# Optimization experiments

Measured on AMD Instinct MI355X. Metric: run time of the kernel, lower is better.

Reference implementation:

```python
import jax, jax.numpy as jnp
import numpy as np

N = 100000   # nodes
E = 1600000  # edges
IN = 128     # input_dim
H = 64       # hidden_dim
OUT = 2      # output_dim
G = 64       # number of graphs in the batch


def setup_inputs() -> dict:
    key = jax.random.key(0)
    ks = jax.random.split(key, 12)
    x = jax.random.normal(ks[0], (N, IN), dtype=jnp.float32)
    edge_index = jax.random.randint(ks[1], (2, E), 0, N, dtype=jnp.int64)
    batch = jnp.sort(jax.random.randint(ks[2], (N,), 0, G, dtype=jnp.int64))
    s = 0.05
    return {
        "x": x,
        "edge_index": edge_index,
        "batch": batch,
        "W1": jax.random.normal(ks[3], (IN, H), dtype=jnp.float32) * s,
        "b1": jnp.zeros((H,), dtype=jnp.float32),
        "W2": jax.random.normal(ks[4], (H, H), dtype=jnp.float32) * s,
        "b2": jnp.zeros((H,), dtype=jnp.float32),
        "W3": jax.random.normal(ks[5], (H, H), dtype=jnp.float32) * s,
        "b3": jnp.zeros((H,), dtype=jnp.float32),
        "Wm1": jax.random.normal(ks[6], (H, H), dtype=jnp.float32) * s,
        "bm1": jnp.zeros((H,), dtype=jnp.float32),
        "Wm2": jax.random.normal(ks[7], (H, OUT), dtype=jnpp.float32) * s if False else jax.random.normal(ks[7], (H, OUT), dtype=jnp.float32) * s,
        "bm2": jnp.zeros((OUT,), dtype=jnp.float32),
    }


def _gcn_conv(x, W, b, src, dst, norm, n_nodes):
    # PyG GCNConv: h = x @ W; message = norm * h[src]; scatter-add at dst; + bias
    h = x @ W                                  # [N, H]
    msg = h[src] * norm[:, None]               # [E+N, H] gather + scale
    out = jax.ops.segment_sum(msg, dst, num_segments=n_nodes)
    return out + b


def reference(x, edge_index, batch, W1, b1, W2, b2, W3, b3, Wm1, bm1, Wm2, bm2):
    n = x.shape[0]
    # add self-loops (PyG GCNConv default add_self_loops=True)
    loop = jnp.arange(n, dtype=edge_index.dtype)
    src = jnp.concatenate([edge_index[0], loop])
    dst = jnp.concatenate([edge_index[1], loop])
    # symmetric normalization deg^-1/2 (deg over target nodes, incl. self-loops)
    deg = jax.ops.segment_sum(jnp.ones_like(dst, dtype=x.dtype), dst, num_segments=n)
    dinv = jnp.where(deg > 0, jax.lax.rsqrt(deg), 0.0)
    norm = dinv[src] * dinv[dst]               # [E+N]

    h = jax.nn.relu(_gcn_conv(x, W1, b1, src, dst, norm, n))   # dropout: eval -> identity
    h = jax.nn.relu(_gcn_conv(h, W2, b2, src, dst, norm, n))
    h = jax.nn.relu(_gcn_conv(h, W3, b3, src, dst, norm, n))

    # global_mean_pool over batch ids
    sums = jax.ops.segment_sum(h, batch, num_segments=G)       # [G, H]
    cnts = jax.ops.segment_sum(jnp.ones((n,), dtype=h.dtype), batch, num_segments=G)
    pooled = sums / jnp.maximum(cnts, 1.0)[:, None]

    # MLP head: Linear -> ReLU -> (Dropout eval) -> Linear
    z = jax.nn.relu(pooled @ Wm1 + bm1)
    return z @ Wm2 + bm2                                       # [G, OUT]
```

## Files before the change

### kernel.cpp

```cpp
#include <hip/hip_runtime.h>
#include <hip/hip_bf16.h>

#define NNODES 100000
#define NEDGES 1600000
#define IND 128
#define HD 64
#define OUTD 2
#define NG 64
#define SCAN_CHUNK 1024
#define BINSHIFT 9
#define BINSZ 512
#define PB 256

typedef __attribute__((ext_vector_type(8))) short short8v;
typedef __attribute__((ext_vector_type(4))) float floatx4;

static __device__ __forceinline__ unsigned short f2bf(float f) {
    __hip_bfloat16 h = __float2bfloat16(f);
    return *(unsigned short*)&h;
}
static __device__ __forceinline__ float bf2f(unsigned short u) {
    __hip_bfloat16 h = *(__hip_bfloat16*)&u;
    return __bfloat162float(h);
}

__global__ __launch_bounds__(256) void binA_kernel(const int* __restrict__ dst,
                                                   int* __restrict__ bbc,
                                                   int E, int nbins) {
    __shared__ int lh[256];
    lh[threadIdx.x] = 0;
    __syncthreads();
    int ebpb = (E + PB - 1) / PB;
    int e0 = blockIdx.x * ebpb;
    int e1 = min(e0 + ebpb, E);
    for (int e = e0 + threadIdx.x; e < e1; e += 256)
        atomicAdd(&lh[dst[e] >> BINSHIFT], 1);
    __syncthreads();
    bbc[blockIdx.x * 256 + threadIdx.x] = lh[threadIdx.x];
}

__global__ __launch_bounds__(256) void binB1_kernel(int* __restrict__ bbc,
                                                    int* __restrict__ binTotal,
                                                    int* __restrict__ binStart) {
    __shared__ int ws[4];
    int b = blockIdx.x;
    int t = threadIdx.x, lane = t & 63, wv = t >> 6;
    int v = bbc[t * 256 + b];
    int sc = v;
#pragma unroll
    for (int d = 1; d < 64; d <<= 1) { int u = __shfl_up(sc, d, 64); if (lane >= d) sc += u; }
    if (lane == 63) ws[wv] = sc;
    __syncthreads();
    int add = 0;
    for (int w = 0; w < wv; w++) add += ws[w];
    bbc[t * 256 + b] = sc - v + add;
    if (t == 255) { int tot = sc + add; binTotal[b] = tot; binStart[b] = tot; }
}

__global__ __launch_bounds__(64) void scan_bsums_kernel(int* __restrict__ bsum, int nchunks) {
    int lane = threadIdx.x;
    int cpl = (nchunks + 63) / 64;
    int vals[8];
    int i0 = lane * cpl;
    int t = 0;
    for (int k = 0; k < cpl; k++) {
        int i = i0 + k;
        vals[k] = (i < nchunks) ? bsum[i] : 0;
        t += vals[k];
    }
    int sc = t;
#pragma unroll
    for (int d = 1; d < 64; d <<= 1) { int v = __shfl_up(sc, d, 64); if (lane >= d) sc += v; }
    int ex = sc - t;
    for (int k = 0; k < cpl; k++) {
        int i = i0 + k;
        if (i < nchunks) bsum[i] = ex;
        ex += vals[k];
    }
}

__global__ __launch_bounds__(256) void binC_kernel(const int* __restrict__ src,
                                                   const int* __restrict__ dst,
                                                   const int* __restrict__ bbc,
                                                   const int* __restrict__ binStart,
                                                   unsigned int* __restrict__ binned,
                                                   int E, int nbins) {
    __shared__ int cur[256];
    int t = threadIdx.x;
    if (t < nbins) cur[t] = binStart[t] + bbc[blockIdx.x * 256 + t];
    __syncthreads();
    int ebpb = (E + PB - 1) / PB;
    int e0 = blockIdx.x * ebpb;
    int e1 = min(e0 + ebpb, E);
    for (int e = e0 + t; e < e1; e += 256) {
        int d = dst[e];
        int b = d >> BINSHIFT;
        int p = atomicAdd(&cur[b], 1);
        binned[p] = ((unsigned int)(d & (BINSZ - 1)) << 17) | (unsigned int)src[e];
    }
}

__global__ __launch_bounds__(256) void binH_kernel(const unsigned int* __restrict__ binned,
                                                   const int* __restrict__ binStart,
                                                   const int* __restrict__ binTotal,
                                                   int* __restrict__ hist,
                                                   float* __restrict__ dinv, int n) {
    __shared__ int dh[BINSZ];
    int b = blockIdx.x;
    int t = threadIdx.x;
    dh[t] = 0; dh[t + 256] = 0;
    __syncthreads();
    int s0 = binStart[b], cnt = binTotal[b];
    for (int i = t; i < cnt; i += 256)
        atomicAdd(&dh[binned[s0 + i] >> 17], 1);
    __syncthreads();
#pragma unroll
    for (int r = 0; r < 2; r++) {
        int i = t + r * 256;
        int node = (b << BINSHIFT) + i;
        if (node < n) {
            int dg = dh[i];
            hist[node] = dg;
            dinv[node] = 1.0f / sqrtf((float)(dg + 1));
        }
    }
}

__global__ __launch_bounds__(256) void scan_sum_kernel(const int* __restrict__ hist,
                                                       int* __restrict__ bsum, int n) {
    __shared__ int wsums[4];
    int lane = threadIdx.x & 63, wv = threadIdx.x >> 6;
    int i0 = blockIdx.x * SCAN_CHUNK + threadIdx.x * 4;
    int t = 0;
#pragma unroll
    for (int k = 0; k < 4; k++) { int i = i0 + k; if (i < n) t += hist[i]; }
#pragma unroll
    for (int d = 32; d > 0; d >>= 1) t += __shfl_down(t, d, 64);
    if (lane == 0) wsums[wv] = t;
    __syncthreads();
    if (threadIdx.x == 0) bsum[blockIdx.x] = wsums[0] + wsums[1] + wsums[2] + wsums[3];
}

__global__ __launch_bounds__(256) void scan_write_kernel(const int* __restrict__ hist,
                                                         const int* __restrict__ bofs,
                                                         int* __restrict__ rowptr,
                                                         int n, int total) {
    __shared__ int wsum[4];
    int lane = threadIdx.x & 63, wv = threadIdx.x >> 6;
    int i0 = blockIdx.x * SCAN_CHUNK + threadIdx.x * 4;
    int h[4]; int t = 0;
#pragma unroll
    for (int k = 0; k < 4; k++) { int i = i0 + k; h[k] = (i < n) ? hist[i] : 0; t += h[k]; }
    int sc = t;
#pragma unroll
    for (int d = 1; d < 64; d <<= 1) { int v = __shfl_up(sc, d, 64); if (lane >= d) sc += v; }
    if (lane == 63) wsum[wv] = sc;
    __syncthreads();
    int wofs = 0;
    for (int w = 0; w < wv; w++) wofs += wsum[w];
    int ex = (sc - t) + wofs + bofs[blockIdx.x];
#pragma unroll
    for (int k = 0; k < 4; k++) { int i = i0 + k; if (i < n) rowptr[i] = ex; ex += h[k]; }
    if (blockIdx.x == 0 && threadIdx.x == 0) rowptr[n] = total;
}

__global__ __launch_bounds__(256) void binD_kernel(const unsigned int* __restrict__ binned,
                                                   const int* __restrict__ binStart,
                                                   const int* __restrict__ binTotal,
                                                   const int* __restrict__ hist,
                                                   const int* __restrict__ rowptr,
                                                   int* __restrict__ ssrc, int n) {
    __shared__ int cntL[BINSZ];
    __shared__ int rpL[BINSZ];
    int b = blockIdx.x;
    int t = threadIdx.x;
#pragma unroll
    for (int r = 0; r < 2; r++) {
        int i = t + r * 256;
        int node = (b << BINSHIFT) + i;
        if (node < n) { cntL[i] = hist[node]; rpL[i] = rowptr[node]; }
    }
    __syncthreads();
    int s0 = binStart[b], cnt = binTotal[b];
    for (int i = t; i < cnt; i += 256) {
        unsigned int rec = binned[s0 + i];
        int doff = rec >> 17;
        int s = rec & 0x1FFFF;
        int idx = atomicSub(&cntL[doff], 1) - 1;
        ssrc[rpL[doff] + idx] = s;
    }
}

__global__ __launch_bounds__(256) void cvtWT_kernel(const float* __restrict__ W,
                                                    unsigned short* __restrict__ WT, int K) {
    int i = blockIdx.x * 256 + threadIdx.x;
    if (i < 64 * K) {
        int n = i / K, k = i - n * K;
        WT[i] = f2bf(W[k * 64 + n]);
    }
}

template <int K, bool BF16IN>
__global__ __launch_bounds__(256) void mm_mfma_kernel(const void* __restrict__ Xv,
                                                      const unsigned short* __restrict__ WT,
                                                      const float* __restrict__ dinv,
                                                      unsigned short* __restrict__ Tb, int nn) {
    const int lane = threadIdx.x & 63;
    const int wv   = threadIdx.x >> 6;
    const int nb   = blockIdx.x * 64 + wv * 16;
    if (nb >= nn) return;
    const int col  = lane & 15;
    const int quad = lane >> 4;
    const int m    = min(nb + col, nn - 1);

    floatx4 acc0 = {0.f, 0.f, 0.f, 0.f};
    floatx4 acc1 = {0.f, 0.f, 0.f, 0.f};
    floatx4 acc2 = {0.f, 0.f, 0.f, 0.f};
    floatx4 acc3 = {0.f, 0.f, 0.f, 0.f};

#pragma unroll
    for (int ks = 0; ks < K; ks += 32) {
        const int k0 = ks + quad * 8;
        short8v a;
        if (BF16IN) {
            a = *(const short8v*)((const unsigned short*)Xv + (size_t)m * K + k0);
        } else {
            const float* xr = (const float*)Xv + (size_t)m * K + k0;
            float4 f0 = *(const float4*)(xr);
            float4 f1 = *(const float4*)(xr + 4);
            a[0] = (short)f2bf(f0.x); a[1] = (short)f2bf(f0.y);
            a[2] = (short)f2bf(f0.z); a[3] = (short)f2bf(f0.w);
            a[4] = (short)f2bf(f1.x); a[5] = (short)f2bf(f1.y);
            a[6] = (short)f2bf(f1.z); a[7] = (short)f2bf(f1.w);
        }
        short8v b0 = *(const short8v*)(WT + (size_t)(0  + col) * K + k0);
        short8v b1 = *(const short8v*)(WT + (size_t)(16 + col) * K + k0);
        short8v b2 = *(const short8v*)(WT + (size_t)(32 + col) * K + k0);
        short8v b3 = *(const short8v*)(WT + (size_t)(48 + col) * K + k0);
        acc0 = __builtin_amdgcn_mfma_f32_16x16x32_bf16(a, b0, acc0, 0, 0, 0);
        acc1 = __builtin_amdgcn_mfma_f32_16x16x32_bf16(a, b1, acc1, 0, 0, 0);
        acc2 = __builtin_amdgcn_mfma_f32_16x16x32_bf16(a, b2, acc2, 0, 0, 0);
        acc3 = __builtin_amdgcn_mfma_f32_16x16x32_bf16(a, b3, acc3, 0, 0, 0);
    }

#pragma unroll
    for (int r = 0; r < 4; r++) {
        int node = nb + quad * 4 + r;
        if (node < nn) {
            float sc = dinv[node];
            unsigned short* o = Tb + (size_t)node * 64 + col;
            o[0]  = f2bf(sc * acc0[r]);
            o[16] = f2bf(sc * acc1[r]);
            o[32] = f2bf(sc * acc2[r]);
            o[48] = f2bf(sc * acc3[r]);
        }
    }
}

__global__ __launch_bounds__(256) void agg_kernel(const unsigned short* __restrict__ Tb,
                                                  const int* __restrict__ rowptr,
                                                  const int* __restrict__ ssrc,
                                                  const float* __restrict__ dinv,
                                                  const float* __restrict__ bias,
                                                  unsigned short* __restrict__ Ob, int nn) {
    int wave = __builtin_amdgcn_readfirstlane((blockIdx.x * 256 + threadIdx.x) >> 6);
    int lane = threadIdx.x & 63;
    if (wave >= nn) return;
    int n = wave;
    float acc = bf2f(Tb[(size_t)n * 64 + lane]);
    int rb = rowptr[n], re = rowptr[n + 1];
    int i = rb;
    for (; i + 16 <= re; i += 16) {
        int s[16];
#pragma unroll
        for (int k = 0; k < 16; k++) s[k] = ssrc[i + k];
        float v[16];
#pragma unroll
        for (int k = 0; k < 16; k++) v[k] = bf2f(Tb[(size_t)s[k] * 64 + lane]);
#pragma unroll
        for (int k = 0; k < 16; k++) acc += v[k];
    }
    for (; i + 4 <= re; i += 4) {
        int s0 = ssrc[i], s1 = ssrc[i + 1], s2 = ssrc[i + 2], s3 = ssrc[i + 3];
        float v0 = bf2f(Tb[(size_t)s0 * 64 + lane]);
        float v1 = bf2f(Tb[(size_t)s1 * 64 + lane]);
        float v2 = bf2f(Tb[(size_t)s2 * 64 + lane]);
        float v3 = bf2f(Tb[(size_t)s3 * 64 + lane]);
        acc += v0; acc += v1; acc += v2; acc += v3;
    }
    for (; i < re; i++)
        acc += bf2f(Tb[(size_t)ssrc[i] * 64 + lane]);
    float o = dinv[n] * acc + bias[lane];
    o = o > 0.f ? o : 0.f;
    Ob[(size_t)n * 64 + lane] = f2bf(o);
}

__global__ __launch_bounds__(256) void pool_kernel(const unsigned short* __restrict__ Hb,
                                                   const int* __restrict__ batch,
                                                   float* __restrict__ pooled,
                                                   float* __restrict__ gcnt, int nn) {
    int wid = (blockIdx.x * 256 + threadIdx.x) >> 6;
    int lane = threadIdx.x & 63;
    int nwaves = (gridDim.x * 256) >> 6;
    int per = (nn + nwaves - 1) / nwaves;
    int n0 = wid * per;
    int n1 = n0 + per; if (n1 > nn) n1 = nn;
    if (n0 >= n1) return;
    int cur = batch[n0];
    float acc = 0.f, cnt = 0.f;
    for (int n = n0; n < n1; ++n) {
        int g = batch[n];
        if (g != cur) {
            atomicAdd(&pooled[cur * 64 + lane], acc);
            if (lane == 0) atomicAdd(&gcnt[cur], cnt);
            acc = 0.f; cnt = 0.f; cur = g;
        }
        acc += bf2f(Hb[(size_t)n * 64 + lane]);
        cnt += 1.f;
    }
    atomicAdd(&pooled[cur * 64 + lane], acc);
    if (lane == 0) atomicAdd(&gcnt[cur], cnt);
}

__global__ __launch_bounds__(256) void head_kernel(const float* __restrict__ pooled,
                                                   const float* __restrict__ gcnt,
                                                   const float* __restrict__ Wm1,
                                                   const float* __restrict__ bm1,
                                                   const float* __restrict__ Wm2,
                                                   const float* __restrict__ bm2,
                                                   float* __restrict__ out) {
    __shared__ float P[NG * 64];
    __shared__ float Z[NG * 64];
    int tid = threadIdx.x;
    for (int i = tid; i < NG * 64; i += 256) {
        int g = i >> 6;
        float c = gcnt[g];
        c = c > 1.f ? c : 1.f;
        P[i] = pooled[i] / c;
    }
    __syncthreads();
    for (int i = tid; i < NG * 64; i += 256) {
        int g = i >> 6, j = i & 63;
        float a = bm1[j];
#pragma unroll 8
        for (int k = 0; k < 64; ++k) a += P[g * 64 + k] * Wm1[k * 64 + j];
        Z[i] = a > 0.f ? a : 0.f;
    }
    __syncthreads();
    for (int i = tid; i < NG * OUTD; i += 256) {
        int g = i / OUTD, o = i % OUTD;
        float a = bm2[o];
#pragma unroll 8
        for (int k = 0; k < 64; ++k) a += Z[g * 64 + k] * Wm2[k * OUTD + o];
        out[i] = a;
    }
}

extern "C" void kernel_launch(void* const* d_in, const int* in_sizes, int n_in,
                              void* d_out, int out_size, void* d_ws, size_t ws_size,
                              hipStream_t stream) {
    const float* x    = (const float*)d_in[0];
    const int*  edge  = (const int*)d_in[1];
    const int*  batch = (const int*)d_in[2];
    const float* W1 = (const float*)d_in[3];
    const float* b1 = (const float*)d_in[4];
    const float* W2 = (const float*)d_in[5];
    const float* b2 = (const float*)d_in[6];
    const float* W3 = (const float*)d_in[7];
    const float* b3 = (const float*)d_in[8];
    const float* Wm1 = (const float*)d_in[9];
    const float* bm1 = (const float*)d_in[10];
    const float* Wm2 = (const float*)d_in[11];
    const float* bm2 = (const float*)d_in[12];

    const int N_ = in_sizes[2];
    const int E_ = in_sizes[1] / 2;
    const int* src = edge;
    const int* dst = edge + E_;
    const int nbins = (N_ + BINSZ - 1) >> BINSHIFT;

    char* w = (char*)d_ws;
    auto alloc = [&](size_t bytes) -> void* {
        void* p = (void*)w;
        w += (bytes + 255) & ~(size_t)255;
        return p;
    };
    float* dinv   = (float*)alloc((size_t)N_ * 4);
    int*   hist   = (int*)alloc((size_t)N_ * 4);
    int*   rowptr = (int*)alloc((size_t)(N_ + 1) * 4);
    int*   bsum   = (int*)alloc(512 * 4);
    int*   bbc    = (int*)alloc((size_t)256 * 256 * 4);
    int*   binTotal = (int*)alloc(256 * 4);
    int*   binStart = (int*)alloc(256 * 4);
    int*   ssrc   = (int*)alloc((size_t)E_ * 4);
    unsigned int* binned = (unsigned int*)alloc((size_t)E_ * 4);
    unsigned short* Tb  = (unsigned short*)alloc((size_t)N_ * 64 * 2);
    unsigned short* hBb = (unsigned short*)alloc((size_t)N_ * 64 * 2);
    unsigned short* WT1 = (unsigned short*)alloc((size_t)64 * IND * 2);
    unsigned short* WT2 = (unsigned short*)alloc((size_t)64 * HD * 2);
    unsigned short* WT3 = (unsigned short*)alloc((size_t)64 * HD * 2);
    float* pooled = (float*)alloc((size_t)(NG * 64 + NG) * 4);
    float* gcnt   = pooled + NG * 64;

    const int nchunks = (N_ + SCAN_CHUNK - 1) / SCAN_CHUNK;

    hipMemsetAsync(pooled, 0, (size_t)(NG * 64 + NG) * 4, stream);

    binA_kernel<<<PB, 256, 0, stream>>>(dst, bbc, E_, nbins);
    binB1_kernel<<<nbins, 256, 0, stream>>>(bbc, binTotal, binStart);
    scan_bsums_kernel<<<1, 64, 0, stream>>>(binStart, nbins);
    binC_kernel<<<PB, 256, 0, stream>>>(src, dst, bbc, binStart, binned, E_, nbins);
    binH_kernel<<<nbins, 256, 0, stream>>>(binned, binStart, binTotal, hist, dinv, N_);
    scan_sum_kernel<<<nchunks, 256, 0, stream>>>(hist, bsum, N_);
    scan_bsums_kernel<<<1, 64, 0, stream>>>(bsum, nchunks);
    scan_write_kernel<<<nchunks, 256, 0, stream>>>(hist, bsum, rowptr, N_, E_);
    binD_kernel<<<nbins, 256, 0, stream>>>(binned, binStart, binTotal, hist, rowptr, ssrc, N_);

    cvtWT_kernel<<<(64 * IND + 255) / 256, 256, 0, stream>>>(W1, WT1, IND);
    cvtWT_kernel<<<(64 * HD + 255) / 256, 256, 0, stream>>>(W2, WT2, HD);
    cvtWT_kernel<<<(64 * HD + 255) / 256, 256, 0, stream>>>(W3, WT3, HD);

    const int mmblk = (N_ + 63) / 64;
    const int aggblk = (N_ + 3) / 4;

    mm_mfma_kernel<IND, false><<<mmblk, 256, 0, stream>>>(x, WT1, dinv, Tb, N_);
    agg_kernel<<<aggblk, 256, 0, stream>>>(Tb, rowptr, ssrc, dinv, b1, hBb, N_);
    mm_mfma_kernel<HD, true><<<mmblk, 256, 0, stream>>>(hBb, WT2, dinv, Tb, N_);
    agg_kernel<<<aggblk, 256, 0, stream>>>(Tb, rowptr, ssrc, dinv, b2, hBb, N_);
    mm_mfma_kernel<HD, true><<<mmblk, 256, 0, stream>>>(hBb, WT3, dinv, Tb, N_);
    agg_kernel<<<aggblk, 256, 0, stream>>>(Tb, rowptr, ssrc, dinv, b3, hBb, N_);

    pool_kernel<<<256, 256, 0, stream>>>(hBb, batch, pooled, gcnt, N_);
    head_kernel<<<1, 256, 0, stream>>>(pooled, gcnt, Wm1, bm1, Wm2, bm2, (float*)d_out);
}
```

Measured before the change: 411.0 us.

## Fuse degree histogram, CSR scan and edge scatter into one per-bin kernel

Since edges are already bucketed by destination bin, and bin offsets are known from binStart, each bin block now computes the degree histogram, a local exclusive scan for rowptr, dinv, and the final scatter of sources into CSR order, all in one kernel. This replaces the separate hist, two-pass global scan and binD kernels, removing several launches and the round trips of hist/rowptr through global memory. The three weight-transpose kernels are also merged into one launch. In exchange, each bin block does more serial work.

```diff
diff --git a/kernel.cpp b/kernel.cpp
--- a/kernel.cpp
+++ b/kernel.cpp
@@ -7,7 +7,6 @@
 #define HD 64
 #define OUTD 2
 #define NG 64
-#define SCAN_CHUNK 1024
 #define BINSHIFT 9
 #define BINSZ 512
 #define PB 256
@@ -100,14 +99,18 @@
     }
 }
 
-__global__ __launch_bounds__(256) void binH_kernel(const unsigned int* __restrict__ binned,
-                                                   const int* __restrict__ binStart,
-                                                   const int* __restrict__ binTotal,
-                                                   int* __restrict__ hist,
-                                                   float* __restrict__ dinv, int n) {
+__global__ __launch_bounds__(256) void binHD_kernel(const unsigned int* __restrict__ binned,
+                                                    const int* __restrict__ binStart,
+                                                    const int* __restrict__ binTotal,
+                                                    float* __restrict__ dinv,
+                                                    int* __restrict__ rowptr,
+                                                    int* __restrict__ ssrc,
+                                                    int n, int E) {
     __shared__ int dh[BINSZ];
-    int b = blockIdx.x;
-    int t = threadIdx.x;
+    __shared__ int rp[BINSZ];
+    __shared__ int wsum[4];
+    int b = blockIdx.x, t = threadIdx.x;
+    int lane = t & 63, wv = t >> 6;
     dh[t] = 0; dh[t + 256] = 0;
     __syncthreads();
     int s0 = binStart[b], cnt = binTotal[b];
@@ -118,85 +121,56 @@
     for (int r = 0; r < 2; r++) {
         int i = t + r * 256;
         int node = (b << BINSHIFT) + i;
-        if (node < n) {
-            int dg = dh[i];
-            hist[node] = dg;
-            dinv[node] = 1.0f / sqrtf((float)(dg + 1));
-        }
-    }
-}
-
-__global__ __launch_bounds__(256) void scan_sum_kernel(const int* __restrict__ hist,
-                                                       int* __restrict__ bsum, int n) {
-    __shared__ int wsums[4];
-    int lane = threadIdx.x & 63, wv = threadIdx.x >> 6;
-    int i0 = blockIdx.x * SCAN_CHUNK + threadIdx.x * 4;
-    int t = 0;
-#pragma unroll
-    for (int k = 0; k < 4; k++) { int i = i0 + k; if (i < n) t += hist[i]; }
-#pragma unroll
-    for (int d = 32; d > 0; d >>= 1) t += __shfl_down(t, d, 64);
-    if (lane == 0) wsums[wv] = t;
-    __syncthreads();
-    if (threadIdx.x == 0) bsum[blockIdx.x] = wsums[0] + wsums[1] + wsums[2] + wsums[3];
-}
-
-__global__ __launch_bounds__(256) void scan_write_kernel(const int* __restrict__ hist,
-                                                         const int* __restrict__ bofs,
-                                                         int* __restrict__ rowptr,
-                                                         int n, int total) {
-    __shared__ int wsum[4];
-    int lane = threadIdx.x & 63, wv = threadIdx.x >> 6;
-    int i0 = blockIdx.x * SCAN_CHUNK + threadIdx.x * 4;
-    int h[4]; int t = 0;
-#pragma unroll
-    for (int k = 0; k < 4; k++) { int i = i0 + k; h[k] = (i < n) ? hist[i] : 0; t += h[k]; }
-    int sc = t;
+        if (node < n) dinv[node] = 1.0f / sqrtf((float)(dh[i] + 1));
+    }
+    int d0 = dh[2 * t], d1 = dh[2 * t + 1];
+    int p = d0 + d1;
+    int sc = p;
 #pragma unroll
     for (int d = 1; d < 64; d <<= 1) { int v = __shfl_up(sc, d, 64); if (lane >= d) sc += v; }
     if (lane == 63) wsum[wv] = sc;
     __syncthreads();
-    int wofs = 0;
-    for (int w = 0; w < wv; w++) wofs += wsum[w];
-    int ex = (sc - t) + wofs + bofs[blockIdx.x];
-#pragma unroll
-    for (int k = 0; k < 4; k++) { int i = i0 + k; if (i < n) rowptr[i] = ex; ex += h[k]; }
-    if (blockIdx.x == 0 && threadIdx.x == 0) rowptr[n] = total;
-}
-
-__global__ __launch_bounds__(256) void binD_kernel(const unsigned int* __restrict__ binned,
-                                                   const int* __restrict__ binStart,
-                                                   const int* __restrict__ binTotal,
-                                                   const int* __restrict__ hist,
-                                                   const int* __restrict__ rowptr,
-                                                   int* __restrict__ ssrc, int n) {
-    __shared__ int cntL[BINSZ];
-    __shared__ int rpL[BINSZ];
-    int b = blockIdx.x;
-    int t = threadIdx.x;
+    int add = 0;
+    for (int w2 = 0; w2 < wv; w2++) add += wsum[w2];
+    int ex = sc - p + add;
+    rp[2 * t]     = ex;
+    rp[2 * t + 1] = ex + d0;
+    __syncthreads();
 #pragma unroll
     for (int r = 0; r < 2; r++) {
         int i = t + r * 256;
         int node = (b << BINSHIFT) + i;
-        if (node < n) { cntL[i] = hist[node]; rpL[i] = rowptr[node]; }
-    }
-    __syncthreads();
-    int s0 = binStart[b], cnt = binTotal[b];
+        if (node < n) rowptr[node] = s0 + rp[i];
+    }
+    if (b == 0 && t == 0) rowptr[n] = E;
+    __syncthreads();
     for (int i = t; i < cnt; i += 256) {
         unsigned int rec = binned[s0 + i];
         int doff = rec >> 17;
         int s = rec & 0x1FFFF;
-        int idx = atomicSub(&cntL[doff], 1) - 1;
-        ssrc[rpL[doff] + idx] = s;
-    }
-}
-
-__global__ __launch_bounds__(256) void cvtWT_kernel(const float* __restrict__ W,
-                                                    unsigned short* __restrict__ WT, int K) {
+        int idx = atomicSub(&dh[doff], 1) - 1;
+        ssrc[s0 + rp[doff] + idx] = s;
+    }
+}
+
+__global__ __launch_bounds__(256) void cvtWT3_kernel(const float* __restrict__ W1,
+                                                     const float* __restrict__ W2,
+                                                     const float* __restrict__ W3,
+                                                     unsigned short* __restrict__ WT1,
+                                                     unsigned short* __restrict__ WT2,
+                                                     unsigned short* __restrict__ WT3) {
     int i = blockIdx.x * 256 + threadIdx.x;
-    if (i < 64 * K) {
-        int n = i / K, k = i - n * K;
-        WT[i] = f2bf(W[k * 64 + n]);
+    if (i < 64 * IND) {
+        int n = i / IND, k = i - n * IND;
+        WT1[i] = f2bf(W1[k * 64 + n]);
+    } else if (i < 64 * IND + 64 * HD) {
+        int j = i - 64 * IND;
+        int n = j / HD, k = j - n * HD;
+        WT2[j] = f2bf(W2[k * 64 + n]);
+    } else if (i < 64 * IND + 2 * 64 * HD) {
+        int j = i - 64 * IND - 64 * HD;
+        int n = j / HD, k = j - n * HD;
+        WT3[j] = f2bf(W3[k * 64 + n]);
     }
 }
 
@@ -386,9 +360,7 @@
         return p;
     };
     float* dinv   = (float*)alloc((size_t)N_ * 4);
-    int*   hist   = (int*)alloc((size_t)N_ * 4);
     int*   rowptr = (int*)alloc((size_t)(N_ + 1) * 4);
-    int*   bsum   = (int*)alloc(512 * 4);
     int*   bbc    = (int*)alloc((size_t)256 * 256 * 4);
     int*   binTotal = (int*)alloc(256 * 4);
     int*   binStart = (int*)alloc(256 * 4);
@@ -402,23 +374,16 @@
     float* pooled = (float*)alloc((size_t)(NG * 64 + NG) * 4);
     float* gcnt   = pooled + NG * 64;
 
-    const int nchunks = (N_ + SCAN_CHUNK - 1) / SCAN_CHUNK;
-
     hipMemsetAsync(pooled, 0, (size_t)(NG * 64 + NG) * 4, stream);
 
     binA_kernel<<<PB, 256, 0, stream>>>(dst, bbc, E_, nbins);
     binB1_kernel<<<nbins, 256, 0, stream>>>(bbc, binTotal, binStart);
     scan_bsums_kernel<<<1, 64, 0, stream>>>(binStart, nbins);
     binC_kernel<<<PB, 256, 0, stream>>>(src, dst, bbc, binStart, binned, E_, nbins);
-    binH_kernel<<<nbins, 256, 0, stream>>>(binned, binStart, binTotal, hist, dinv, N_);
-    scan_sum_kernel<<<nchunks, 256, 0, stream>>>(hist, bsum, N_);
-    scan_bsums_kernel<<<1, 64, 0, stream>>>(bsum, nchunks);
-    scan_write_kernel<<<nchunks, 256, 0, stream>>>(hist, bsum, rowptr, N_, E_);
-    binD_kernel<<<nbins, 256, 0, stream>>>(binned, binStart, binTotal, hist, rowptr, ssrc, N_);
-
-    cvtWT_kernel<<<(64 * IND + 255) / 256, 256, 0, stream>>>(W1, WT1, IND);
-    cvtWT_kernel<<<(64 * HD + 255) / 256, 256, 0, stream>>>(W2, WT2, HD);
-    cvtWT_kernel<<<(64 * HD + 255) / 256, 256, 0, stream>>>(W3, WT3, HD);
+    binHD_kernel<<<nbins, 256, 0, stream>>>(binned, binStart, binTotal, dinv, rowptr, ssrc, N_, E_);
+
+    cvtWT3_kernel<<<(64 * IND + 2 * 64 * HD + 255) / 256, 256, 0, stream>>>(
+        W1, W2, W3, WT1, WT2, WT3);
 
     const int mmblk = (N_ + 63) / 64;
     const int aggblk = (N_ + 3) / 4;
```

New measurement: 396.5 us. 3.5% less time.
